# Optimization experiments

Hardware: AMD Instinct MI355X
Metric: run time of the kernel (lower is better)

The kernel has to match this reference:

```python
import jax, jax.numpy as jnp
import numpy as np

EDGES = np.array([[0,6],[0,5],[6,8],[5,7],[0,62],[62,63],[63,64],[59,64],[59,60],[60,61],[61,62],[0,74],[71,72],[72,73],[73,74],[74,75],[75,76],[76,77],[77,78],[78,79],[79,80],[80,81],[81,82],[71,82],[71,83],[77,87],[83,84],[84,85],[85,86],[86,87],[87,88],[88,89],[89,90],[83,90],[0,65],[65,66],[66,67],[67,68],[68,69],[69,70],[65,70],[7,91],[91,92],[92,93],[93,94],[94,95],[91,96],[96,97],[97,98],[98,99],[91,100],[100,101],[101,102],[102,103],[91,104],[104,105],[105,106],[106,107],[91,108],[108,109],[109,110],[110,111],[8,112],[112,113],[113,114],[114,115],[115,116],[112,117],[117,118],[118,119],[119,120],[112,121],[121,122],[122,123],[123,124],[112,125],[125,126],[126,127],[127,128],[112,129],[129,130],[130,131],[131,132]], dtype=np.int32)
N_NODES = 102


def _gcn_structure():
    # Keep only edges whose endpoints fit in the 102-node feature view,
    # add self-loops, and compute symmetric GCN normalization (PyG gcn_norm).
    keep = (EDGES[:, 0] < N_NODES) & (EDGES[:, 1] < N_NODES)
    e = EDGES[keep]
    row, col = e[:, 0], e[:, 1]
    loops = np.arange(N_NODES, dtype=np.int32)
    row_f = np.concatenate([row, loops])
    col_f = np.concatenate([col, loops])
    deg = np.zeros(N_NODES, dtype=np.float32)
    np.add.at(deg, col_f, 1.0)  # in-degree incl. self-loop
    dinv = 1.0 / np.sqrt(np.maximum(deg, 1.0))
    norm = (dinv[row_f] * dinv[col_f]).astype(np.float32)
    return row_f, col_f, norm

_ROW, _COL, _NORM = _gcn_structure()


def setup_inputs() -> dict:
    key = jax.random.key(0)
    ks = jax.random.split(key, 5)
    B = 8192
    return {
        "x": jax.random.normal(ks[0], (B, 204), dtype=jnp.float32),
        "W_gcn": jax.random.normal(ks[1], (2, 64), dtype=jnp.float32) * 0.5,
        "b_gcn": jax.random.normal(ks[2], (64,), dtype=jnp.float32) * 0.1,
        "W_proj": jax.random.normal(ks[3], (64, 128), dtype=jnp.float32) * 0.1,
        "b_proj": jax.random.normal(ks[4], (128,), dtype=jnp.float32) * 0.1,
    }


def reference(x, W_gcn, b_gcn, W_proj, b_proj):
    B = x.shape[0]
    xn = x.reshape(B, N_NODES, 2)                      # (B, 102, 2)
    h = jnp.einsum('bni,ih->bnh', xn, W_gcn)           # GCN linear: (B, 102, H)
    norm = jnp.asarray(_NORM)
    msgs = h[:, _ROW, :] * norm[None, :, None]         # gather + normalize: (B, E+N, H)
    agg = jnp.zeros_like(h).at[:, _COL, :].add(msgs)   # scatter-add into targets
    agg = agg + b_gcn                                  # GCN bias
    act = jax.nn.relu(agg)                             # activation
    out = jnp.einsum('bnh,he->bne', act, W_proj) + b_proj  # projection: (B, 102, 128)
    return out
```

## Files before the change

### kernel.cpp

```cpp
#include <hip/hip_runtime.h>
#include <hip/hip_bf16.h>

#define NN   102
#define NE   83
#define NPAD 128

using bf16x8 = __attribute__((ext_vector_type(8))) short;
using f32x4  = __attribute__((ext_vector_type(4))) float;

__device__ __constant__ int EDGES_C[NE * 2] = {
    0,6, 0,5, 6,8, 5,7, 0,62, 62,63, 63,64, 59,64, 59,60, 60,61, 61,62,
    0,74, 71,72, 72,73, 73,74, 74,75, 75,76, 76,77, 77,78, 78,79, 79,80,
    80,81, 81,82, 71,82, 71,83, 77,87, 83,84, 84,85, 85,86, 86,87, 87,88,
    88,89, 89,90, 83,90, 0,65, 65,66, 66,67, 67,68, 68,69, 69,70, 65,70,
    7,91, 91,92, 92,93, 93,94, 94,95, 91,96, 96,97, 97,98, 98,99, 91,100,
    100,101, 101,102, 102,103, 91,104, 104,105, 105,106, 106,107, 91,108,
    108,109, 109,110, 110,111, 8,112, 112,113, 113,114, 114,115, 115,116,
    112,117, 117,118, 118,119, 119,120, 112,121, 121,122, 122,123, 123,124,
    112,125, 125,126, 126,127, 127,128, 112,129, 129,130, 130,131, 131,132
};

#define WS_BFRAG 0
#define WS_OFF   16384
#define WS_ER    (16384 + 512)
#define WS_EN    (16384 + 512 + 1024)

__device__ inline unsigned short f2bf(float f) {
  union { float f; unsigned u; } v; v.f = f;
  unsigned r = v.u + 0x7fffu + ((v.u >> 16) & 1u);
  return (unsigned short)(r >> 16);
}

__device__ inline unsigned cvt_pk_bf16(float lo, float hi) {
  unsigned r;
  asm("v_cvt_pk_bf16_f32 %0, %1, %2" : "=v"(r) : "v"(lo), "v"(hi));
  return r;
}

__global__ void gnn_setup(const float* __restrict__ Wp, char* __restrict__ ws) {
  __shared__ float s_dinv[NN];
  __shared__ int   s_cnt[NN];
  __shared__ int   s_off[NN + 1];
  const int t = threadIdx.x;

  if (t < NN) {
    int deg = 1, cnt = 1;
    for (int e = 0; e < NE; ++e) {
      int r = EDGES_C[2*e], c = EDGES_C[2*e+1];
      if (r < NN && c == t) { ++deg; ++cnt; }
    }
    s_dinv[t] = 1.0f / sqrtf((float)deg);
    s_cnt[t]  = cnt;
  }
  __syncthreads();
  if (t < NN) {
    int o = 0;
    for (int c = 0; c < t; ++c) o += s_cnt[c];
    s_off[t] = o;
    if (t == NN - 1) s_off[NN] = o + s_cnt[t];
  }
  __syncthreads();
  int*   off = (int*)(ws + WS_OFF);
  int*   er  = (int*)(ws + WS_ER);
  float* en  = (float*)(ws + WS_EN);
  if (t < NN) {
    int c = t, pos = s_off[c];
    float dc = s_dinv[c];
    er[pos] = c; en[pos] = dc * dc; ++pos;
    for (int e = 0; e < NE; ++e) {
      int r = EDGES_C[2*e], cc = EDGES_C[2*e+1];
      if (r < NN && cc == c) { er[pos] = r; en[pos] = s_dinv[r] * dc; ++pos; }
    }
    off[c] = s_off[c];
    if (c == 0) off[NN] = s_off[NN];
  }
  unsigned short* bf = (unsigned short*)(ws + WS_BFRAG);
  for (int idx = t; idx < 16 * 64; idx += blockDim.x) {
    int lane = idx & 63;
    int f    = idx >> 6;
    int mt   = f >> 1, kc = f & 1;
    int e    = mt * 16 + (lane & 15);
    int kb   = kc * 32 + (lane >> 4) * 8;
    unsigned short* dst = bf + idx * 8;
#pragma unroll
    for (int i = 0; i < 8; ++i) dst[i] = f2bf(Wp[(kb + i) * 128 + e]);
  }
}

__global__ __launch_bounds__(256) void gnn_main(
    const float* __restrict__ x, const float* __restrict__ Wg,
    const float* __restrict__ bg, const float* __restrict__ bp,
    const char* __restrict__ ws, float* __restrict__ out) {
  const int b    = blockIdx.x;
  const int t    = threadIdx.x;
  const int lane = t & 63;
  const int wv   = t >> 6;

  __shared__ float sx[204];
  __shared__ float sy[NPAD][2];
  __shared__ float swg[128];
  __shared__ float sbg[64];
  __shared__ float sbp[128];
  __shared__ float st[4][16][132];

  if (t < 204) sx[t] = x[(size_t)b * 204 + t];
  if (t < 128) { swg[t] = Wg[t]; sbp[t] = bp[t]; }
  if (t < 64)  sbg[t] = bg[t];
  __syncthreads();

  if (t < NPAD) {
    float y0 = 0.f, y1 = 0.f;
    if (t < NN) {
      const int*   off = (const int*)(ws + WS_OFF);
      const int*   er  = (const int*)(ws + WS_ER);
      const float* en  = (const float*)(ws + WS_EN);
      int s = off[t], e2 = off[t + 1];
      for (int j = s; j < e2; ++j) {
        int r = er[j]; float w = en[j];
        y0 = fmaf(w, sx[2 * r],     y0);
        y1 = fmaf(w, sx[2 * r + 1], y1);
      }
    }
    sy[t][0] = y0; sy[t][1] = y1;
  }
  __syncthreads();

  const int l15 = lane & 15;
  const int lhi = lane >> 4;
  const int kb  = lhi * 8;
  const int rb  = lhi * 4;

  bf16x8 Bact[2][2];
#pragma unroll
  for (int nl = 0; nl < 2; ++nl)
#pragma unroll
    for (int kc = 0; kc < 2; ++kc) {
      bf16x8 z = {0,0,0,0,0,0,0,0};
      Bact[nl][kc] = z;
    }

  const int nt0 = wv * 2;
#pragma unroll
  for (int nl = 0; nl < 2; ++nl) {
    const int nt = nt0 + nl;
    if (nt >= 7) continue;
    const int node = nt * 16 + l15;
    const float y0 = sy[node][0], y1 = sy[node][1];
#pragma unroll
    for (int kc = 0; kc < 2; ++kc) {
      float v[8];
#pragma unroll
      for (int i = 0; i < 8; ++i) {
        int h = kc * 32 + kb + i;
        float a = fmaf(y0, swg[h], fmaf(y1, swg[64 + h], sbg[h]));
        v[i] = fmaxf(a, 0.f);
      }
      union { unsigned u[4]; bf16x8 f; } pk;
      pk.u[0] = cvt_pk_bf16(v[0], v[1]);
      pk.u[1] = cvt_pk_bf16(v[2], v[3]);
      pk.u[2] = cvt_pk_bf16(v[4], v[5]);
      pk.u[3] = cvt_pk_bf16(v[6], v[7]);
      Bact[nl][kc] = pk.f;
    }
  }

  const bf16x8* bfr = (const bf16x8*)(ws + WS_BFRAG);
  bf16x8 Apf[8][2];
#pragma unroll
  for (int mt = 0; mt < 8; ++mt) {
    Apf[mt][0] = bfr[(mt * 2 + 0) * 64 + lane];
    Apf[mt][1] = bfr[(mt * 2 + 1) * 64 + lane];
  }

  f32x4 acc[8][2];
#pragma unroll
  for (int mt = 0; mt < 8; ++mt) {
    f32x4 bb = *(const f32x4*)&sbp[mt * 16 + rb];
    acc[mt][0] = bb;
    acc[mt][1] = bb;
  }

#pragma unroll
  for (int mt = 0; mt < 8; ++mt)
#pragma unroll
    for (int nl = 0; nl < 2; ++nl) {
      if (nt0 + nl >= 7) continue;
#pragma unroll
      for (int kc = 0; kc < 2; ++kc)
        acc[mt][nl] = __builtin_amdgcn_mfma_f32_16x16x32_bf16(
            Apf[mt][kc], Bact[nl][kc], acc[mt][nl], 0, 0, 0);
    }

  const int c32 = (lane & 31) * 4;
  const int rhi = lane >> 5;
#pragma unroll
  for (int nl = 0; nl < 2; ++nl) {
    const int nt = nt0 + nl;
    if (nt >= 7) continue;
#pragma unroll
    for (int mt = 0; mt < 8; ++mt)
      *(f32x4*)&st[wv][l15][mt * 16 + rb] = acc[mt][nl];
#pragma unroll
    for (int pass = 0; pass < 8; ++pass) {
      const int n2   = pass * 2 + rhi;
      const int node = nt * 16 + n2;
      if (node < NN) {
        f32x4 row = *(const f32x4*)&st[wv][n2][c32];
        *(f32x4*)(out + ((size_t)b * NN + node) * 128 + c32) = row;
      }
    }
  }
}

extern "C" void kernel_launch(void* const* d_in, const int* in_sizes, int n_in,
                              void* d_out, int out_size, void* d_ws, size_t ws_size,
                              hipStream_t stream) {
  const float* x  = (const float*)d_in[0];
  const float* Wg = (const float*)d_in[1];
  const float* bg = (const float*)d_in[2];
  const float* Wp = (const float*)d_in[3];
  const float* bp = (const float*)d_in[4];
  float* out = (float*)d_out;
  const int B = in_sizes[0] / 204;

  gnn_setup<<<1, 256, 0, stream>>>(Wp, (char*)d_ws);
  gnn_main<<<B, 256, 0, stream>>>(x, Wg, bg, bp, (const char*)d_ws, out);
}
```

Baseline: 118.5 us.

## Map one batch sample per wavefront instead of one per block

Each 256-thread block now processes four samples, one per wavefront, and each wave runs the GCN aggregation and all seven node tiles of the projection on its own. This removes the block-wide barrier after aggregation, loads the projection weight fragments once per sample per wave rather than once per wave per tile pair, and cuts the grid to a quarter. The trade-off is that each wave works through its seven tiles one after another, so there is less parallelism inside a sample, and x is now read with vector loads.

```diff
diff --git a/kernel.cpp b/kernel.cpp
--- a/kernel.cpp
+++ b/kernel.cpp
@@ -90,62 +90,76 @@
 __global__ __launch_bounds__(256) void gnn_main(
     const float* __restrict__ x, const float* __restrict__ Wg,
     const float* __restrict__ bg, const float* __restrict__ bp,
-    const char* __restrict__ ws, float* __restrict__ out) {
-  const int b    = blockIdx.x;
+    const char* __restrict__ ws, float* __restrict__ out, int B) {
   const int t    = threadIdx.x;
   const int lane = t & 63;
   const int wv   = t >> 6;
-
-  __shared__ float sx[204];
-  __shared__ float sy[NPAD][2];
+  const int b    = blockIdx.x * 4 + wv;
+
   __shared__ float swg[128];
   __shared__ float sbg[64];
   __shared__ float sbp[128];
+  __shared__ float sxw[4][208];
+  __shared__ float syw[4][NPAD][2];
   __shared__ float st[4][16][132];
 
-  if (t < 204) sx[t] = x[(size_t)b * 204 + t];
   if (t < 128) { swg[t] = Wg[t]; sbp[t] = bp[t]; }
   if (t < 64)  sbg[t] = bg[t];
   __syncthreads();
 
-  if (t < NPAD) {
-    float y0 = 0.f, y1 = 0.f;
-    if (t < NN) {
-      const int*   off = (const int*)(ws + WS_OFF);
-      const int*   er  = (const int*)(ws + WS_ER);
-      const float* en  = (const float*)(ws + WS_EN);
-      int s = off[t], e2 = off[t + 1];
-      for (int j = s; j < e2; ++j) {
-        int r = er[j]; float w = en[j];
-        y0 = fmaf(w, sx[2 * r],     y0);
-        y1 = fmaf(w, sx[2 * r + 1], y1);
+  if (b >= B) return;
+
+  float* sx = sxw[wv];
+  float (*sy)[2] = syw[wv];
+
+  if (lane < 51)
+    *(f32x4*)&sx[lane * 4] = *(const f32x4*)(x + (size_t)b * 204 + lane * 4);
+
+  {
+    const int*   off = (const int*)(ws + WS_OFF);
+    const int*   er  = (const int*)(ws + WS_ER);
+    const float* en  = (const float*)(ws + WS_EN);
+#pragma unroll
+    for (int half = 0; half < 2; ++half) {
+      const int n = lane + half * 64;
+      float y0 = 0.f, y1 = 0.f;
+      if (n < NN) {
+        int s = off[n], e2 = off[n + 1];
+        for (int j = s; j < e2; ++j) {
+          int r = er[j]; float w = en[j];
+          y0 = fmaf(w, sx[2 * r],     y0);
+          y1 = fmaf(w, sx[2 * r + 1], y1);
+        }
       }
-    }
-    sy[t][0] = y0; sy[t][1] = y1;
-  }
-  __syncthreads();
+      sy[n][0] = y0; sy[n][1] = y1;
+    }
+  }
 
   const int l15 = lane & 15;
   const int lhi = lane >> 4;
   const int kb  = lhi * 8;
   const int rb  = lhi * 4;
-
-  bf16x8 Bact[2][2];
-#pragma unroll
-  for (int nl = 0; nl < 2; ++nl)
-#pragma unroll
-    for (int kc = 0; kc < 2; ++kc) {
-      bf16x8 z = {0,0,0,0,0,0,0,0};
-      Bact[nl][kc] = z;
-    }
-
-  const int nt0 = wv * 2;
-#pragma unroll
-  for (int nl = 0; nl < 2; ++nl) {
-    const int nt = nt0 + nl;
-    if (nt >= 7) continue;
+  const int c32 = (lane & 31) * 4;
+  const int rhi = lane >> 5;
+
+  const bf16x8* bfr = (const bf16x8*)(ws + WS_BFRAG);
+  bf16x8 Apf[8][2];
+#pragma unroll
+  for (int mt = 0; mt < 8; ++mt) {
+    Apf[mt][0] = bfr[(mt * 2 + 0) * 64 + lane];
+    Apf[mt][1] = bfr[(mt * 2 + 1) * 64 + lane];
+  }
+  f32x4 bias[8];
+#pragma unroll
+  for (int mt = 0; mt < 8; ++mt)
+    bias[mt] = *(const f32x4*)&sbp[mt * 16 + rb];
+
+  float* ob = out + (size_t)b * (NN * 128);
+
+  for (int nt = 0; nt < 7; ++nt) {
     const int node = nt * 16 + l15;
     const float y0 = sy[node][0], y1 = sy[node][1];
+    bf16x8 Bact[2];
 #pragma unroll
     for (int kc = 0; kc < 2; ++kc) {
       float v[8];
@@ -160,53 +174,30 @@
       pk.u[1] = cvt_pk_bf16(v[2], v[3]);
       pk.u[2] = cvt_pk_bf16(v[4], v[5]);
       pk.u[3] = cvt_pk_bf16(v[6], v[7]);
-      Bact[nl][kc] = pk.f;
-    }
-  }
-
-  const bf16x8* bfr = (const bf16x8*)(ws + WS_BFRAG);
-  bf16x8 Apf[8][2];
-#pragma unroll
-  for (int mt = 0; mt < 8; ++mt) {
-    Apf[mt][0] = bfr[(mt * 2 + 0) * 64 + lane];
-    Apf[mt][1] = bfr[(mt * 2 + 1) * 64 + lane];
-  }
-
-  f32x4 acc[8][2];
-#pragma unroll
-  for (int mt = 0; mt < 8; ++mt) {
-    f32x4 bb = *(const f32x4*)&sbp[mt * 16 + rb];
-    acc[mt][0] = bb;
-    acc[mt][1] = bb;
-  }
-
-#pragma unroll
-  for (int mt = 0; mt < 8; ++mt)
-#pragma unroll
-    for (int nl = 0; nl < 2; ++nl) {
-      if (nt0 + nl >= 7) continue;
+      Bact[kc] = pk.f;
+    }
+
+    f32x4 acc[8];
+#pragma unroll
+    for (int mt = 0; mt < 8; ++mt) acc[mt] = bias[mt];
+#pragma unroll
+    for (int mt = 0; mt < 8; ++mt)
 #pragma unroll
       for (int kc = 0; kc < 2; ++kc)
-        acc[mt][nl] = __builtin_amdgcn_mfma_f32_16x16x32_bf16(
-            Apf[mt][kc], Bact[nl][kc], acc[mt][nl], 0, 0, 0);
-    }
-
-  const int c32 = (lane & 31) * 4;
-  const int rhi = lane >> 5;
-#pragma unroll
-  for (int nl = 0; nl < 2; ++nl) {
-    const int nt = nt0 + nl;
-    if (nt >= 7) continue;
+        acc[mt] = __builtin_amdgcn_mfma_f32_16x16x32_bf16(
+            Apf[mt][kc], Bact[kc], acc[mt], 0, 0, 0);
+
 #pragma unroll
     for (int mt = 0; mt < 8; ++mt)
-      *(f32x4*)&st[wv][l15][mt * 16 + rb] = acc[mt][nl];
+      *(f32x4*)&st[wv][l15][mt * 16 + rb] = acc[mt];
+
+    const int rows = (nt < 6) ? 16 : (NN - 96);
 #pragma unroll
     for (int pass = 0; pass < 8; ++pass) {
-      const int n2   = pass * 2 + rhi;
-      const int node = nt * 16 + n2;
-      if (node < NN) {
+      const int n2 = pass * 2 + rhi;
+      if (n2 < rows) {
         f32x4 row = *(const f32x4*)&st[wv][n2][c32];
-        *(f32x4*)(out + ((size_t)b * NN + node) * 128 + c32) = row;
+        *(f32x4*)(ob + (nt * 16 + n2) * 128 + c32) = row;
       }
     }
   }
@@ -224,5 +215,5 @@
   const int B = in_sizes[0] / 204;
 
   gnn_setup<<<1, 256, 0, stream>>>(Wp, (char*)d_ws);
-  gnn_main<<<B, 256, 0, stream>>>(x, Wg, bg, bp, (const char*)d_ws, out);
-}
+  gnn_main<<<(B + 3) / 4, 256, 0, stream>>>(x, Wg, bg, bp, (const char*)d_ws, out, B);
+}
```

After: 108.9 us. 1.09x faster.
